# Optimization experiments

Hardware: AMD Instinct MI355X
Metric: run time of the kernel (lower is better)

The kernel has to match this reference:

```python
import jax, jax.numpy as jnp
import numpy as np

HEADS = 4
DIM_HEAD = 32
SCALE = DIM_HEAD ** -0.5
EPS = 1e-5


def setup_inputs() -> dict:
    key = jax.random.key(0)
    k1, k2, k3, k4 = jax.random.split(key, 4)
    dim = 256
    hidden = HEADS * DIM_HEAD  # 128
    x = jax.random.normal(k1, (16, dim, 64, 64), dtype=jnp.float32)
    # 1x1 conv weights stored as [out_ch, in_ch] (kernel size 1 squeezed)
    w_qkv = jax.random.normal(k2, (hidden * 3, dim), dtype=jnp.float32) * (dim ** -0.5)
    w_out = jax.random.normal(k3, (dim, hidden), dtype=jnp.float32) * (hidden ** -0.5)
    b_out = jax.random.normal(k4, (dim,), dtype=jnp.float32) * 0.01
    g = jnp.ones((1, dim, 1, 1), dtype=jnp.float32)  # LayerNorm gain
    return {"x": x, "w_qkv": w_qkv, "w_out": w_out, "b_out": b_out, "g": g}


def reference(x, w_qkv, w_out, b_out, g):
    b, c, h, w = x.shape
    n = h * w
    # 1x1 conv to qkv: [b, 3*hidden, h, w]
    qkv = jnp.einsum('oc,bchw->bohw', w_qkv, x)
    q, k, v = jnp.split(qkv, 3, axis=1)

    def to_heads(t):
        return t.reshape(b, HEADS, DIM_HEAD, n)  # b h d n

    q, k, v = to_heads(q), to_heads(k), to_heads(v)
    q = jax.nn.softmax(q, axis=2) * SCALE       # softmax over head-dim d
    k = jax.nn.softmax(k, axis=3)               # softmax over spatial n
    v = v / n                                    # v / (h*w)
    context = jnp.einsum('bhdn,bhen->bhde', k, v)
    out = jnp.einsum('bhde,bhdn->bhen', context, q)  # b h e n
    out = out.reshape(b, HEADS * DIM_HEAD, h, w)
    # output 1x1 conv with bias
    out = jnp.einsum('oc,bchw->bohw', w_out, out) + b_out[None, :, None, None]
    # channel LayerNorm (biased variance over dim=1)
    mean = jnp.mean(out, axis=1, keepdims=True)
    var = jnp.var(out, axis=1, keepdims=True)
    return (out - mean) * jax.lax.rsqrt(var + EPS) * g
```

## Files before the change

### kernel.cpp

```cpp
#include <hip/hip_runtime.h>

typedef short short8 __attribute__((ext_vector_type(8)));
typedef float f32x16 __attribute__((ext_vector_type(16)));
typedef unsigned short ushort_t;

#define B_    16
#define C_    256
#define N_    4096
#define H_    4
#define HID_  128
#define SCALE_ 0.17677669529663687f
#define EPS_  1e-5f

__device__ inline ushort_t f2bf(float f) {
  union { float f; unsigned u; } a; a.f = f;
  unsigned r = a.u + 0x7FFFu + ((a.u >> 16) & 1u);
  return (ushort_t)(r >> 16);
}

__device__ inline int2 pack4(float a, float b, float c, float d) {
  int2 o;
  o.x = (int)f2bf(a) | ((int)f2bf(b) << 16);
  o.y = (int)f2bf(c) | ((int)f2bf(d) << 16);
  return o;
}

__device__ inline short8 ld_frag16(const ushort_t* p) {
  return __builtin_bit_cast(short8, *(const int4*)p);
}
__device__ inline short8 ld_frag8(const ushort_t* p) {
  int2 a = *(const int2*)p, b = *(const int2*)(p + 4);
  int4 t; t.x = a.x; t.y = a.y; t.z = b.x; t.w = b.y;
  return __builtin_bit_cast(short8, t);
}

__global__ void k0_wswz(const float* __restrict__ w, ushort_t* __restrict__ wsw) {
  int gid = blockIdx.x * 256 + threadIdx.x;
  int ln = gid & 63, kc = (gid >> 6) & 15, mt = gid >> 10;
  int row = mt * 32 + (ln & 31);
  int col = kc * 16 + (ln >> 5) * 8;
  const float* src = w + (size_t)row * 256 + col;
  float4 a = *(const float4*)src, b = *(const float4*)(src + 4);
  union { ushort_t u[8]; int4 v; } o;
  o.u[0] = f2bf(a.x); o.u[1] = f2bf(a.y); o.u[2] = f2bf(a.z); o.u[3] = f2bf(a.w);
  o.u[4] = f2bf(b.x); o.u[5] = f2bf(b.y); o.u[6] = f2bf(b.z); o.u[7] = f2bf(b.w);
  *(int4*)(wsw + (size_t)gid * 8) = o.v;
}

__global__ __launch_bounds__(256, 3) void k1_qkv(
    const float* __restrict__ x, const ushort_t* __restrict__ wsw,
    ushort_t* __restrict__ qp, float* __restrict__ pctx, float* __restrict__ psum)
{
  __shared__ __align__(16) union {
    ushort_t Xs[64 * 264];
    struct { ushort_t kt[128 * 68]; ushort_t vt[128 * 68]; } s2;
  } sm;

  const int tid = threadIdx.x;
  const int b = blockIdx.y;
  const int blk = blockIdx.x;
  const int n0 = blk * 64;
  const int hw = tid >> 6, lane = tid & 63;
  const int half = lane >> 5, lm = lane & 31;

  {
    const float* xsrc = x + (size_t)b * C_ * N_ + n0;
    const int n4 = tid & 15;
    const int cq0 = tid >> 4;
    #pragma unroll
    for (int cc = 0; cc < 4; ++cc) {
      const int cq = cq0 + cc * 16;
      const float* p = xsrc + (size_t)(cq * 4) * N_ + n4 * 4;
      float4 a0 = *(const float4*)(p);
      float4 a1 = *(const float4*)(p + N_);
      float4 a2 = *(const float4*)(p + 2 * N_);
      float4 a3 = *(const float4*)(p + 3 * N_);
      ushort_t* d = sm.Xs + (((cq >> 1) ^ n4) * 8 + (cq & 1) * 4) + (n4 * 4) * 264;
      *(int2*)(d + 0 * 264) = pack4(a0.x, a1.x, a2.x, a3.x);
      *(int2*)(d + 1 * 264) = pack4(a0.y, a1.y, a2.y, a3.y);
      *(int2*)(d + 2 * 264) = pack4(a0.z, a1.z, a2.z, a3.z);
      *(int2*)(d + 3 * 264) = pack4(a0.w, a1.w, a2.w, a3.w);
    }
  }
  __syncthreads();

  f32x16 acc0a, acc0b, acc1a, acc1b, acc2a, acc2b;
  for (int r = 0; r < 16; ++r) {
    acc0a[r] = 0.0f; acc0b[r] = 0.0f; acc1a[r] = 0.0f;
    acc1b[r] = 0.0f; acc2a[r] = 0.0f; acc2b[r] = 0.0f;
  }
  {
    const ushort_t* xrow0 = sm.Xs + lm * 264;
    const ushort_t* xrow1 = sm.Xs + (32 + lm) * 264;
    const int sn0 = lm >> 2;
    const int sn1 = 8 + (lm >> 2);
    const ushort_t* wl = wsw + (size_t)(hw * 16 * 64 + lane) * 8;
    #pragma unroll
    for (int kc = 0; kc < 16; ++kc) {
      short8 b0 = ld_frag16(xrow0 + (((2 * kc + half) ^ sn0) << 3));
      short8 b1 = ld_frag16(xrow1 + (((2 * kc + half) ^ sn1) << 3));
      short8 af0 = ld_frag16(wl + kc * 512);
      short8 af1 = ld_frag16(wl + 32768 + kc * 512);
      short8 af2 = ld_frag16(wl + 65536 + kc * 512);
      acc0a = __builtin_amdgcn_mfma_f32_32x32x16_bf16(af0, b0, acc0a, 0, 0, 0);
      acc0b = __builtin_amdgcn_mfma_f32_32x32x16_bf16(af0, b1, acc0b, 0, 0, 0);
      acc1a = __builtin_amdgcn_mfma_f32_32x32x16_bf16(af1, b0, acc1a, 0, 0, 0);
      acc1b = __builtin_amdgcn_mfma_f32_32x32x16_bf16(af1, b1, acc1b, 0, 0, 0);
      acc2a = __builtin_amdgcn_mfma_f32_32x32x16_bf16(af2, b0, acc2a, 0, 0, 0);
      acc2b = __builtin_amdgcn_mfma_f32_32x32x16_bf16(af2, b1, acc2b, 0, 0, 0);
    }
  }

  {
    ushort_t* qpb = qp + (size_t)b * N_ * 128;
    {
      float m = -1e30f;
      for (int r = 0; r < 16; ++r) m = fmaxf(m, acc0a[r]);
      m = fmaxf(m, __shfl_xor(m, 32));
      float qe[16]; float s = 0.0f;
      for (int r = 0; r < 16; ++r) { qe[r] = __expf(acc0a[r] - m); s += qe[r]; }
      s += __shfl_xor(s, 32);
      float sc = SCALE_ / s;
      const int gnt = blk * 2;
      for (int q = 0; q < 4; ++q) {
        int kc = hw * 2 + (q >> 1);
        int fl = (q & 1) * 32 + lm;
        int2 o = pack4(qe[q * 4 + 0] * sc, qe[q * 4 + 1] * sc,
                       qe[q * 4 + 2] * sc, qe[q * 4 + 3] * sc);
        *(int2*)(qpb + (size_t)((gnt * 8 + kc) * 64 + fl) * 8 + 4 * half) = o;
      }
    }
    {
      float m = -1e30f;
      for (int r = 0; r < 16; ++r) m = fmaxf(m, acc0b[r]);
      m = fmaxf(m, __shfl_xor(m, 32));
      float qe[16]; float s = 0.0f;
      for (int r = 0; r < 16; ++r) { qe[r] = __expf(acc0b[r] - m); s += qe[r]; }
      s += __shfl_xor(s, 32);
      float sc = SCALE_ / s;
      const int gnt = blk * 2 + 1;
      for (int q = 0; q < 4; ++q) {
        int kc = hw * 2 + (q >> 1);
        int fl = (q & 1) * 32 + lm;
        int2 o = pack4(qe[q * 4 + 0] * sc, qe[q * 4 + 1] * sc,
                       qe[q * 4 + 2] * sc, qe[q * 4 + 3] * sc);
        *(int2*)(qpb + (size_t)((gnt * 8 + kc) * 64 + fl) * 8 + 4 * half) = o;
      }
    }
  }

  __syncthreads();

  for (int r = 0; r < 16; ++r) {
    int row = (r & 3) + 8 * (r >> 2) + 4 * half;
    ushort_t* krow = sm.s2.kt + (hw * 32 + row) * 68;
    ushort_t* vrow = sm.s2.vt + (hw * 32 + row) * 68;
    krow[lm]      = f2bf(__expf(acc1a[r]));
    krow[32 + lm] = f2bf(__expf(acc1b[r]));
    vrow[lm]      = f2bf(acc2a[r]);
    vrow[32 + lm] = f2bf(acc2b[r]);
  }
  __syncthreads();

  {
    f32x16 cacc, sacc;
    for (int r = 0; r < 16; ++r) { cacc[r] = 0.0f; sacc[r] = 0.0f; }
    short8 ones;
    #pragma unroll
    for (int j = 0; j < 8; ++j) ones[j] = (short)0x3F80;
    const ushort_t* ka = sm.s2.kt + (hw * 32 + lm) * 68 + half * 8;
    const ushort_t* va = sm.s2.vt + (hw * 32 + lm) * 68 + half * 8;
    #pragma unroll
    for (int ks = 0; ks < 4; ++ks) {
      short8 af = ld_frag8(ka + ks * 16);
      short8 bf = ld_frag8(va + ks * 16);
      cacc = __builtin_amdgcn_mfma_f32_32x32x16_bf16(af, bf, cacc, 0, 0, 0);
      sacc = __builtin_amdgcn_mfma_f32_32x32x16_bf16(af, ones, sacc, 0, 0, 0);
    }
    float* pc = pctx + ((size_t)(b * 4 + hw) * 64 + blk) * 1024;
    for (int r = 0; r < 16; ++r) {
      int row = (r & 3) + 8 * (r >> 2) + 4 * half;
      pc[row * 32 + lm] = cacc[r];
    }
    if (lm == 0) {
      float* ps = psum + ((size_t)(b * 4 + hw) * 64 + blk) * 32;
      for (int r = 0; r < 16; ++r) {
        int row = (r & 3) + 8 * (r >> 2) + 4 * half;
        ps[row] = sacc[r];
      }
    }
  }
}

__global__ __launch_bounds__(256) void krw(
    const float* __restrict__ pctx, const float* __restrict__ psum,
    const float* __restrict__ wout, ushort_t* __restrict__ weff)
{
  __shared__ float ctxs[32][32];
  __shared__ float inv[32];
  __shared__ float red[8][32];
  const int tid = threadIdx.x;
  const int bh = blockIdx.x;
  const int pb = bh >> 2, ph = bh & 3;

  {
    const int d = tid & 31, part = tid >> 5;
    const float* ps = psum + (size_t)bh * 2048 + part * 8 * 32 + d;
    float t = 0.0f;
    #pragma unroll
    for (int g = 0; g < 8; ++g) t += ps[g * 32];
    red[part][d] = t;
  }
  float4 s4 = make_float4(0.f, 0.f, 0.f, 0.f);
  {
    const float* pc = pctx + (size_t)bh * 65536 + tid * 4;
    #pragma unroll 8
    for (int c = 0; c < 64; ++c) {
      float4 v = *(const float4*)(pc + c * 1024);
      s4.x += v.x; s4.y += v.y; s4.z += v.z; s4.w += v.w;
    }
  }
  __syncthreads();
  if (tid < 32) {
    float u = 0.0f;
    #pragma unroll
    for (int p = 0; p < 8; ++p) u += red[p][tid];
    inv[tid] = 1.0f / (u * 4096.0f);
  }
  __syncthreads();
  {
    float iv = inv[tid >> 3];
    float* crow = &ctxs[0][0] + tid * 4;
    crow[0] = s4.x * iv; crow[1] = s4.y * iv; crow[2] = s4.z * iv; crow[3] = s4.w * iv;
  }
  __syncthreads();
  {
    const int oc = tid;
    const int mt = oc >> 5, lmm = oc & 31;
    const float* wrow = wout + (size_t)oc * HID_ + ph * 32;
    float wr[32];
    for (int e = 0; e < 32; ++e) wr[e] = wrow[e];
    float vals[32];
    for (int d = 0; d < 32; ++d) {
      float s = 0.0f;
      for (int e = 0; e < 32; ++e) s += wr[e] * ctxs[d][e];
      vals[d] = s;
    }
    ushort_t* wb_b = weff + (size_t)pb * 32768;
    for (int kci = 0; kci < 2; ++kci) {
      int kc = ph * 2 + kci;
      for (int hf = 0; hf < 2; ++hf) {
        int d0 = kci * 16 + hf * 8;
        union { ushort_t u[8]; int4 v; } o;
        for (int j = 0; j < 8; ++j) o.u[j] = f2bf(vals[d0 + j]);
        *(int4*)(wb_b + (size_t)((mt * 8 + kc) * 64 + hf * 32 + lmm) * 8) = o.v;
      }
    }
  }
}

__global__ __launch_bounds__(256, 4) void k3_out(
    const ushort_t* __restrict__ weff, const ushort_t* __restrict__ qp,
    const float* __restrict__ bout, const float* __restrict__ g,
    float* __restrict__ out)
{
  __shared__ float part_s[2][64], part_s2[2][64];
  __shared__ float st_mu[64], st_rs[64];

  const int tid = threadIdx.x;
  const int b = blockIdx.y;
  const int blk = blockIdx.x;
  const int n0 = blk * 64;
  const int w = tid >> 6, lane = tid & 63;
  const int half = lane >> 5, lm = lane & 31;
  const int ntile = w & 1, mgrp = w >> 1;
  const int gnt = blk * 2 + ntile;

  f32x16 acc[4];
  for (int i = 0; i < 4; ++i)
    for (int r = 0; r < 16; ++r) acc[i][r] = 0.0f;

  {
    const ushort_t* qb = qp + (size_t)b * N_ * 128 + (size_t)gnt * 8 * 64 * 8;
    const ushort_t* wbase = weff + (size_t)b * 32768 + ((size_t)(mgrp * 4) * 8 * 64 + lane) * 8;
    for (int kc = 0; kc < 8; ++kc) {
      short8 bfrag = ld_frag16(qb + (size_t)(kc * 64 + lane) * 8);
      for (int i = 0; i < 4; ++i) {
        short8 af = ld_frag16(wbase + (size_t)((i * 8 + kc) * 64) * 8);
        acc[i] = __builtin_amdgcn_mfma_f32_32x32x16_bf16(af, bfrag, acc[i], 0, 0, 0);
      }
    }
  }

  float s = 0.0f, s2v = 0.0f;
  for (int i = 0; i < 4; ++i) {
    int mt = mgrp * 4 + i;
    for (int r = 0; r < 16; ++r) {
      int row = mt * 32 + (r & 3) + 8 * (r >> 2) + 4 * half;
      acc[i][r] += bout[row];
      float v = acc[i][r];
      s += v; s2v += v * v;
    }
  }
  s += __shfl_xor(s, 32);
  s2v += __shfl_xor(s2v, 32);
  if (half == 0) { part_s[mgrp][ntile * 32 + lm] = s; part_s2[mgrp][ntile * 32 + lm] = s2v; }
  __syncthreads();
  if (tid < 64) {
    float S = part_s[0][tid] + part_s[1][tid];
    float S2 = part_s2[0][tid] + part_s2[1][tid];
    float mu = S * (1.0f / 256.0f);
    float var = S2 * (1.0f / 256.0f) - mu * mu;
    st_mu[tid] = mu;
    st_rs[tid] = rsqrtf(var + EPS_);
  }
  __syncthreads();

  const int col = ntile * 32 + lm;
  const float mu = st_mu[col];
  const float rs = st_rs[col];
  float* ob = out + (size_t)b * C_ * N_ + n0 + col;
  for (int i = 0; i < 4; ++i) {
    int mt = mgrp * 4 + i;
    for (int r = 0; r < 16; ++r) {
      int row = mt * 32 + (r & 3) + 8 * (r >> 2) + 4 * half;
      ob[(size_t)row * N_] = (acc[i][r] - mu) * rs * g[row];
    }
  }
}

extern "C" void kernel_launch(void* const* d_in, const int* in_sizes, int n_in,
                              void* d_out, int out_size, void* d_ws, size_t ws_size,
                              hipStream_t stream) {
  (void)in_sizes; (void)n_in; (void)out_size; (void)ws_size;
  const float* x    = (const float*)d_in[0];
  const float* wqkv = (const float*)d_in[1];
  const float* wout = (const float*)d_in[2];
  const float* bout = (const float*)d_in[3];
  const float* g    = (const float*)d_in[4];
  float* out = (float*)d_out;

  char* ws = (char*)d_ws;
  ushort_t* qp    = (ushort_t*)(ws);
  float*    pctx  = (float*)(ws + ((size_t)16 << 20));
  float*    psum  = (float*)(ws + ((size_t)32 << 20));
  ushort_t* weff  = (ushort_t*)(ws + ((size_t)32 << 20) + (512 << 10));
  ushort_t* wsw   = (ushort_t*)(ws + ((size_t)33 << 20) + (512 << 10));

  k0_wswz<<<48, 256, 0, stream>>>(wqkv, wsw);
  k1_qkv<<<dim3(64, 16), 256, 0, stream>>>(x, wsw, qp, pctx, psum);
  krw<<<64, 256, 0, stream>>>(pctx, psum, wout, weff);
  k3_out<<<dim3(64, 16), 256, 0, stream>>>(weff, qp, bout, g, out);
}
```

Before: 159.9 us.

## Overlap second half of x staging with first-half QKV MFMA; nontemporal output stores

The x tile load into LDS is split in two halves. Channels 0–127 are staged first. The global loads and LDS writes for channels 128–255 are then interleaved with the first eight MFMA k-steps, with a barrier before the remaining k-steps. The aim is to hide global-load latency behind tensor-core work instead of stalling on the full tile up front, at the cost of an extra barrier and more live registers. The final LayerNorm output writes now use nontemporal stores, which are meant to avoid polluting the cache with streaming output.

```diff
diff --git a/kernel.cpp b/kernel.cpp
--- a/kernel.cpp
+++ b/kernel.cpp
@@ -63,24 +63,32 @@
   const int hw = tid >> 6, lane = tid & 63;
   const int half = lane >> 5, lm = lane & 31;
 
-  {
-    const float* xsrc = x + (size_t)b * C_ * N_ + n0;
-    const int n4 = tid & 15;
-    const int cq0 = tid >> 4;
-    #pragma unroll
-    for (int cc = 0; cc < 4; ++cc) {
-      const int cq = cq0 + cc * 16;
-      const float* p = xsrc + (size_t)(cq * 4) * N_ + n4 * 4;
-      float4 a0 = *(const float4*)(p);
-      float4 a1 = *(const float4*)(p + N_);
-      float4 a2 = *(const float4*)(p + 2 * N_);
-      float4 a3 = *(const float4*)(p + 3 * N_);
-      ushort_t* d = sm.Xs + (((cq >> 1) ^ n4) * 8 + (cq & 1) * 4) + (n4 * 4) * 264;
-      *(int2*)(d + 0 * 264) = pack4(a0.x, a1.x, a2.x, a3.x);
-      *(int2*)(d + 1 * 264) = pack4(a0.y, a1.y, a2.y, a3.y);
-      *(int2*)(d + 2 * 264) = pack4(a0.z, a1.z, a2.z, a3.z);
-      *(int2*)(d + 3 * 264) = pack4(a0.w, a1.w, a2.w, a3.w);
-    }
+  const float* xsrc = x + (size_t)b * C_ * N_ + n0;
+  const int n4 = tid & 15;
+  const int cq0 = tid >> 4;
+
+#define STAGE_LOAD(cc, A0, A1, A2, A3) { \
+    const int cq = cq0 + (cc) * 16; \
+    const float* p = xsrc + (size_t)(cq * 4) * N_ + n4 * 4; \
+    A0 = *(const float4*)(p); \
+    A1 = *(const float4*)(p + N_); \
+    A2 = *(const float4*)(p + 2 * N_); \
+    A3 = *(const float4*)(p + 3 * N_); }
+
+#define STAGE_WRITE(cc, A0, A1, A2, A3) { \
+    const int cq = cq0 + (cc) * 16; \
+    ushort_t* d = sm.Xs + (((cq >> 1) ^ n4) * 8 + (cq & 1) * 4) + (n4 * 4) * 264; \
+    *(int2*)(d + 0 * 264) = pack4(A0.x, A1.x, A2.x, A3.x); \
+    *(int2*)(d + 1 * 264) = pack4(A0.y, A1.y, A2.y, A3.y); \
+    *(int2*)(d + 2 * 264) = pack4(A0.z, A1.z, A2.z, A3.z); \
+    *(int2*)(d + 3 * 264) = pack4(A0.w, A1.w, A2.w, A3.w); }
+
+  {
+    float4 a0, a1, a2, a3, b0, b1, b2, b3;
+    STAGE_LOAD(0, a0, a1, a2, a3);
+    STAGE_LOAD(1, b0, b1, b2, b3);
+    STAGE_WRITE(0, a0, a1, a2, a3);
+    STAGE_WRITE(1, b0, b1, b2, b3);
   }
   __syncthreads();
 
@@ -89,27 +97,43 @@
     acc0a[r] = 0.0f; acc0b[r] = 0.0f; acc1a[r] = 0.0f;
     acc1b[r] = 0.0f; acc2a[r] = 0.0f; acc2b[r] = 0.0f;
   }
-  {
-    const ushort_t* xrow0 = sm.Xs + lm * 264;
-    const ushort_t* xrow1 = sm.Xs + (32 + lm) * 264;
-    const int sn0 = lm >> 2;
-    const int sn1 = 8 + (lm >> 2);
-    const ushort_t* wl = wsw + (size_t)(hw * 16 * 64 + lane) * 8;
-    #pragma unroll
-    for (int kc = 0; kc < 16; ++kc) {
-      short8 b0 = ld_frag16(xrow0 + (((2 * kc + half) ^ sn0) << 3));
-      short8 b1 = ld_frag16(xrow1 + (((2 * kc + half) ^ sn1) << 3));
-      short8 af0 = ld_frag16(wl + kc * 512);
-      short8 af1 = ld_frag16(wl + 32768 + kc * 512);
-      short8 af2 = ld_frag16(wl + 65536 + kc * 512);
-      acc0a = __builtin_amdgcn_mfma_f32_32x32x16_bf16(af0, b0, acc0a, 0, 0, 0);
-      acc0b = __builtin_amdgcn_mfma_f32_32x32x16_bf16(af0, b1, acc0b, 0, 0, 0);
-      acc1a = __builtin_amdgcn_mfma_f32_32x32x16_bf16(af1, b0, acc1a, 0, 0, 0);
-      acc1b = __builtin_amdgcn_mfma_f32_32x32x16_bf16(af1, b1, acc1b, 0, 0, 0);
-      acc2a = __builtin_amdgcn_mfma_f32_32x32x16_bf16(af2, b0, acc2a, 0, 0, 0);
-      acc2b = __builtin_amdgcn_mfma_f32_32x32x16_bf16(af2, b1, acc2b, 0, 0, 0);
-    }
-  }
+  const ushort_t* xrow0 = sm.Xs + lm * 264;
+  const ushort_t* xrow1 = sm.Xs + (32 + lm) * 264;
+  const int sn0 = lm >> 2;
+  const int sn1 = 8 + (lm >> 2);
+  const ushort_t* wl = wsw + (size_t)(hw * 16 * 64 + lane) * 8;
+
+#define GEMM_STEP(kc) { \
+    short8 bb0 = ld_frag16(xrow0 + (((2 * (kc) + half) ^ sn0) << 3)); \
+    short8 bb1 = ld_frag16(xrow1 + (((2 * (kc) + half) ^ sn1) << 3)); \
+    short8 af0 = ld_frag16(wl + (kc) * 512); \
+    short8 af1 = ld_frag16(wl + 32768 + (kc) * 512); \
+    short8 af2 = ld_frag16(wl + 65536 + (kc) * 512); \
+    acc0a = __builtin_amdgcn_mfma_f32_32x32x16_bf16(af0, bb0, acc0a, 0, 0, 0); \
+    acc0b = __builtin_amdgcn_mfma_f32_32x32x16_bf16(af0, bb1, acc0b, 0, 0, 0); \
+    acc1a = __builtin_amdgcn_mfma_f32_32x32x16_bf16(af1, bb0, acc1a, 0, 0, 0); \
+    acc1b = __builtin_amdgcn_mfma_f32_32x32x16_bf16(af1, bb1, acc1b, 0, 0, 0); \
+    acc2a = __builtin_amdgcn_mfma_f32_32x32x16_bf16(af2, bb0, acc2a, 0, 0, 0); \
+    acc2b = __builtin_amdgcn_mfma_f32_32x32x16_bf16(af2, bb1, acc2b, 0, 0, 0); }
+
+  {
+    float4 a0, a1, a2, a3;
+    STAGE_LOAD(2, a0, a1, a2, a3);
+    GEMM_STEP(0); GEMM_STEP(1); GEMM_STEP(2); GEMM_STEP(3);
+    STAGE_WRITE(2, a0, a1, a2, a3);
+    float4 b0, b1, b2, b3;
+    STAGE_LOAD(3, b0, b1, b2, b3);
+    GEMM_STEP(4); GEMM_STEP(5); GEMM_STEP(6); GEMM_STEP(7);
+    STAGE_WRITE(3, b0, b1, b2, b3);
+  }
+  __syncthreads();
+
+  GEMM_STEP(8);  GEMM_STEP(9);  GEMM_STEP(10); GEMM_STEP(11);
+  GEMM_STEP(12); GEMM_STEP(13); GEMM_STEP(14); GEMM_STEP(15);
+
+#undef GEMM_STEP
+#undef STAGE_LOAD
+#undef STAGE_WRITE
 
   {
     ushort_t* qpb = qp + (size_t)b * N_ * 128;
@@ -324,7 +348,7 @@
     int mt = mgrp * 4 + i;
     for (int r = 0; r < 16; ++r) {
       int row = mt * 32 + (r & 3) + 8 * (r >> 2) + 4 * half;
-      ob[(size_t)row * N_] = (acc[i][r] - mu) * rs * g[row];
+      __builtin_nontemporal_store((acc[i][r] - mu) * rs * g[row], ob + (size_t)row * N_);
     }
   }
 }
```

Measured after the change: 165.3 us. 3.3% more time.
